# Kernel optimization log

Measured on AMD Instinct MI355X. Metric: run time of the kernel, lower is better.

Reference implementation:

```python
import jax, jax.numpy as jnp
import numpy as np

EPS = 1e-6
NEG = -10000.0
B, T, V, D, H, L, F = 2, 1024, 32000, 1024, 16, 4, 2730
DH = D // H
SCALE = 1.0 / np.sqrt(DH)


def alibi_slopes(n_head):
    # standard ALiBi geometric slopes (n_head is a power of 2 here)
    start = 2.0 ** (-8.0 / n_head)
    return jnp.asarray([start ** (i + 1) for i in range(n_head)], dtype=jnp.float32)


def rational_softmax(x, eps=EPS):
    # exp-free softmax: Pade [0/2] rational surrogate of exp on shifted (<=0) scores
    s = x - jnp.max(x, axis=-1, keepdims=True)
    num = 1.0 / (1.0 - s + 0.5 * s * s)
    return num / (jnp.sum(num, axis=-1, keepdims=True) + eps)


def me_norm(x, w, eps=EPS):
    # mean-error norm: x / (mean|x| + eps) * w
    return x / (jnp.mean(jnp.abs(x), axis=-1, keepdims=True) + eps) * w


def setup_inputs() -> dict:
    key = jax.random.key(0)
    ks = jax.random.split(key, 9)
    std = 0.02
    return {
        "input_ids": jax.random.randint(ks[0], (B, T), 0, V),
        "embed_w":   jax.random.normal(ks[1], (V, D), jnp.float32) * std,  # tied with head
        "qkv_w":     jax.random.normal(ks[2], (L, 3 * D, D), jnp.float32) * std,
        "out_w":     jax.random.normal(ks[3], (L, D, D), jnp.float32) * std,
        "gate_w":    jax.random.normal(ks[4], (L, 2 * F, D), jnp.float32) * std,
        "wout_w":    jax.random.normal(ks[5], (L, D, F), jnp.float32) * std,
        "norm1_w":   jnp.ones((L, D), jnp.float32),
        "norm2_w":   jnp.ones((L, D), jnp.float32),
        "normf_w":   jnp.ones((D,), jnp.float32),
    }


def _forward(input_ids, embed_w, qkv_w, out_w, gate_w, wout_w, norm1_w, norm2_w, normf_w):
    slopes = alibi_slopes(H)                       # [H]
    pos = jnp.arange(T)
    rel = jnp.abs(pos[:, None] - pos[None, :]).astype(jnp.float32)  # [T,T]
    alibi = -rel[None] * slopes[:, None, None]     # [H,T,T]
    causal = jnp.triu(jnp.ones((T, T), bool), k=1) # future positions

    x = embed_w[input_ids]                         # [B,T,D]

    def block(x, p):
        w_qkv, w_out, w_gate, w_wout, n1, n2 = p
        h = me_norm(x, n1)
        qkv = (h @ w_qkv.T).reshape(B, T, 3, H, DH).transpose(2, 0, 3, 1, 4)
        q, k, v = qkv[0], qkv[1], qkv[2]           # [B,H,T,DH]
        scores = jnp.einsum('bhtd,bhsd->bhts', q, k) * SCALE + alibi
        scores = jnp.where(causal[None, None], NEG, scores)
        probs = rational_softmax(scores)
        o = jnp.einsum('bhts,bhsd->bhtd', probs, v)
        o = o.transpose(0, 2, 1, 3).reshape(B, T, D)
        x = x + o @ w_out.T
        h = me_norm(x, n2)
        gv = h @ w_gate.T                           # [B,T,2F]
        gate, val = gv[..., :F], gv[..., F:]
        sigma = 0.5 * (gate / (jnp.abs(gate) + 1.0) + 1.0)  # rational sigmoid
        x = x + (gate * sigma * val) @ w_wout.T
        return x, None

    x, _ = jax.lax.scan(block, x, (qkv_w, out_w, gate_w, wout_w, norm1_w, norm2_w))
    x = me_norm(x, normf_w)
    logits = x @ embed_w.T                          # tied head, [B,T,V]
    return logits


def reference(input_ids, embed_w, qkv_w, out_w, gate_w, wout_w, norm1_w, norm2_w, normf_w):
    return _forward(input_ids, embed_w, qkv_w, out_w, gate_w, wout_w, norm1_w, norm2_w, normf_w)
```

## Files before the change

### kernel.cpp

```cpp
#include <hip/hip_runtime.h>
#include <math.h>

typedef __attribute__((ext_vector_type(8))) short bf16x8;
typedef __attribute__((ext_vector_type(4))) float f32x4;

namespace {
constexpr int Bc = 2, Tc = 1024, Dc = 1024, Hc = 16, Fc = 2730;
constexpr int Fp = 2752;
constexpr int Gp = 5504;
constexpr int Mc = Bc * Tc;
constexpr float EPSc = 1e-6f;
constexpr float NEGc = -10000.0f;
constexpr float SCALEc = 0.125f;
}

__device__ __forceinline__ unsigned short f2b(float f) {
    unsigned int u = __float_as_uint(f);
    u += 0x7FFFu + ((u >> 16) & 1u);
    return (unsigned short)(u >> 16);
}

__global__ void k_embed(const int* __restrict__ ids, const float* __restrict__ ew,
                        float* __restrict__ x) {
    int row = blockIdx.x;
    int id = ids[row];
    const float4* src = (const float4*)(ew + (size_t)id * Dc);
    float4* dst = (float4*)(x + (size_t)row * Dc);
    dst[threadIdx.x] = src[threadIdx.x];
}

__global__ void k_conv(const float* __restrict__ in, unsigned short* __restrict__ out) {
    size_t i = ((size_t)blockIdx.x * 256 + threadIdx.x) * 4;
    float4 v = *(const float4*)(in + i);
    ushort4 o;
    o.x = f2b(v.x); o.y = f2b(v.y); o.z = f2b(v.z); o.w = f2b(v.w);
    *(ushort4*)(out + i) = o;
}

__global__ void k_conv_gate_ilv(const float* __restrict__ in, unsigned short* __restrict__ out) {
    int r = blockIdx.x;
    int c = threadIdx.x * 4;
    ushort4 o;
    if (r < 2 * Fc) {
        int src = (r >> 1) + (r & 1) * Fc;
        float4 v = *(const float4*)(in + (size_t)src * Dc + c);
        o.x = f2b(v.x); o.y = f2b(v.y); o.z = f2b(v.z); o.w = f2b(v.w);
    } else {
        o.x = o.y = o.z = o.w = 0;
    }
    *(ushort4*)(out + (size_t)r * Dc + c) = o;
}

__global__ void k_conv_padk(const float* __restrict__ in, unsigned short* __restrict__ out) {
    int r = blockIdx.x;
    for (int c = threadIdx.x; c < Fp; c += 256) {
        float v = (c < Fc) ? in[(size_t)r * Fc + c] : 0.0f;
        out[(size_t)r * Fp + c] = f2b(v);
    }
}

__global__ void k_menorm_b(const float* __restrict__ x, const float* __restrict__ w,
                           unsigned short* __restrict__ out) {
    int row = blockIdx.x;
    float4 v = ((const float4*)(x + (size_t)row * Dc))[threadIdx.x];
    float s = fabsf(v.x) + fabsf(v.y) + fabsf(v.z) + fabsf(v.w);
#pragma unroll
    for (int m = 32; m >= 1; m >>= 1) s += __shfl_xor(s, m);
    __shared__ float ws4[4];
    if ((threadIdx.x & 63) == 0) ws4[threadIdx.x >> 6] = s;
    __syncthreads();
    float tot = ws4[0] + ws4[1] + ws4[2] + ws4[3];
    float inv = 1.0f / (tot / (float)Dc + EPSc);
    float4 wv = ((const float4*)w)[threadIdx.x];
    ushort4 o;
    o.x = f2b(v.x * inv * wv.x);
    o.y = f2b(v.y * inv * wv.y);
    o.z = f2b(v.z * inv * wv.z);
    o.w = f2b(v.w * inv * wv.w);
    ((ushort4*)(out + (size_t)row * Dc))[threadIdx.x] = o;
}

template <int MODE, int BM>
__global__ __launch_bounds__(256) void k_mfma_gemm(
    const unsigned short* __restrict__ A, const unsigned short* __restrict__ Bw,
    const float* __restrict__ Res, float* __restrict__ C,
    unsigned short* __restrict__ U0, unsigned short* __restrict__ U1,
    unsigned short* __restrict__ U2, int N, int K) {
    constexpr int MFR = BM / 32;
    __shared__ __align__(16) unsigned short As[BM * 64];
    __shared__ __align__(16) unsigned short Bs[128 * 64];
    const int tid = threadIdx.x;
    const int lane = tid & 63;
    const int wid = tid >> 6;
    const int wr = wid >> 1, wc = wid & 1;
    const int l15 = lane & 15, g = lane >> 4;

    const int nwg = gridDim.x * gridDim.y;
    int w = blockIdx.y * gridDim.x + blockIdx.x;
    int f = (nwg & 7) ? w : ((w & 7) * (nwg >> 3) + (w >> 3));
    const int bm = (f % gridDim.x) * BM, bn = (f / gridDim.x) * 128;

    f32x4 acc[MFR][4] = {};

    const int nk = K >> 6;
    for (int kt = 0; kt < nk; ++kt) {
        const int k0 = kt << 6;
#pragma unroll
        for (int it = 0; it < MFR; ++it) {
            int ci = it * 256 + tid;
            int r = ci >> 3;
            int sc = (ci & 7) ^ (r & 7);
            __builtin_amdgcn_global_load_lds(
                (const __attribute__((address_space(1))) void*)(A + (size_t)(bm + r) * K + k0 + sc * 8),
                (__attribute__((address_space(3))) void*)(As + ci * 8), 16, 0, 0);
        }
#pragma unroll
        for (int it = 0; it < 4; ++it) {
            int ci = it * 256 + tid;
            int r = ci >> 3;
            int sc = (ci & 7) ^ (r & 7);
            __builtin_amdgcn_global_load_lds(
                (const __attribute__((address_space(1))) void*)(Bw + (size_t)(bn + r) * K + k0 + sc * 8),
                (__attribute__((address_space(3))) void*)(Bs + ci * 8), 16, 0, 0);
        }
        __syncthreads();
#pragma unroll
        for (int kk = 0; kk < 2; ++kk) {
            bf16x8 af[MFR], bfr[4];
            const int kc = kk * 4 + g;
#pragma unroll
            for (int m = 0; m < MFR; ++m) {
                int row = wr * (BM / 2) + m * 16 + l15;
                af[m] = *(const bf16x8*)&As[(row * 8 + (kc ^ (row & 7))) * 8];
            }
#pragma unroll
            for (int n = 0; n < 4; ++n) {
                int col = wc * 64 + n * 16 + l15;
                bfr[n] = *(const bf16x8*)&Bs[(col * 8 + (kc ^ (col & 7))) * 8];
            }
#pragma unroll
            for (int m = 0; m < MFR; ++m)
#pragma unroll
                for (int n = 0; n < 4; ++n)
                    acc[m][n] = __builtin_amdgcn_mfma_f32_16x16x32_bf16(af[m], bfr[n], acc[m][n], 0, 0, 0);
        }
        __syncthreads();
    }

#pragma unroll
    for (int m = 0; m < MFR; ++m) {
        int row0 = bm + wr * (BM / 2) + m * 16 + (g << 2);
#pragma unroll
        for (int n = 0; n < 4; ++n) {
            int col = bn + wc * 64 + n * 16 + l15;
            if constexpr (MODE == 0 || MODE == 1) {
#pragma unroll
                for (int j = 0; j < 4; ++j) {
                    size_t idx = (size_t)(row0 + j) * N + col;
                    float v = acc[m][n][j];
                    if (MODE == 1) v += Res[idx];
                    C[idx] = v;
                }
            } else if constexpr (MODE == 2) {
                if (col < 2048) {
                    unsigned short* dst = (col < 1024) ? U0 : U1;
                    int hh = (col & 1023) >> 6, dh = col & 63;
#pragma unroll
                    for (int j = 0; j < 4; ++j) {
                        int row = row0 + j;
                        int b = row >> 10, t = row & 1023;
                        dst[((size_t)((b * Hc + hh) * Tc + t)) * 64 + dh] = f2b(acc[m][n][j]);
                    }
                } else {
                    int hh = (col >> 6) & 15, dh = col & 63;
                    int b = row0 >> 10, t = row0 & 1023;
                    ushort4 o4;
                    o4.x = f2b(acc[m][n][0]); o4.y = f2b(acc[m][n][1]);
                    o4.z = f2b(acc[m][n][2]); o4.w = f2b(acc[m][n][3]);
                    *(ushort4*)&U2[((size_t)((b * Hc + hh) * 64 + dh)) * Tc + t] = o4;
                }
            } else {
                float pv[4];
#pragma unroll
                for (int j = 0; j < 4; ++j) pv[j] = __shfl_xor(acc[m][n][j], 1);
                if ((l15 & 1) == 0) {
                    int fq = col >> 1;
#pragma unroll
                    for (int j = 0; j < 4; ++j) {
                        float gate = acc[m][n][j], val = pv[j];
                        float sigma = 0.5f * (gate / (fabsf(gate) + 1.0f) + 1.0f);
                        U0[(size_t)(row0 + j) * Fp + fq] = f2b(gate * sigma * val);
                    }
                }
            }
        }
    }
}

__global__ __launch_bounds__(512, 2) void k_gemm_8ph(
    const unsigned short* __restrict__ A, const unsigned short* __restrict__ Bw,
    float* __restrict__ C, int N, int K) {
    __shared__ __align__(16) unsigned short As[2][256 * 64];
    __shared__ __align__(16) unsigned short Bs[2][256 * 64];
    const int tid = threadIdx.x;
    const int lane = tid & 63, wid = tid >> 6;
    const int wm = wid >> 2, wn = wid & 3;
    const int l15 = lane & 15, g = lane >> 4;

    const int bm = blockIdx.x * 256;
    const int bn = blockIdx.y * 256;

    const int nk = K >> 6;
    f32x4 acc[8][4] = {};

#define STAGE8(buf, kt)                                                                          \
    {                                                                                            \
        _Pragma("unroll") for (int it = 0; it < 4; ++it) {                                       \
            int ci = it * 512 + tid;                                                             \
            int r = ci >> 3, c = (ci & 7) ^ (r & 7);                                             \
            __builtin_amdgcn_global_load_lds(                                                    \
                (const __attribute__((address_space(1))) void*)(A + (size_t)(bm + r) * K + (kt) * 64 + c * 8), \
                (__attribute__((address_space(3))) void*)(&As[buf][ci * 8]), 16, 0, 0);          \
        }                                                                                        \
        _Pragma("unroll") for (int it = 0; it < 4; ++it) {                                       \
            int ci = it * 512 + tid;                                                             \
            int r = ci >> 3, c = (ci & 7) ^ (r & 7);                                             \
            __builtin_amdgcn_global_load_lds(                                                    \
                (const __attribute__((address_space(1))) void*)(Bw + (size_t)(bn + r) * K + (kt) * 64 + c * 8), \
                (__attribute__((address_space(3))) void*)(&Bs[buf][ci * 8]), 16, 0, 0);          \
        }                                                                                        \
    }

    STAGE8(0, 0);
    STAGE8(1, 1);
    asm volatile("s_waitcnt vmcnt(8)" ::: "memory");
    __builtin_amdgcn_s_barrier();

    for (int kt = 0; kt < nk; ++kt) {
        const int buf = kt & 1;
        const unsigned short* Ab = As[buf];
        const unsigned short* Bb = Bs[buf];
        bf16x8 bfr[4][2];
#pragma unroll
        for (int n = 0; n < 4; ++n) {
            int col = wn * 64 + n * 16 + l15;
#pragma unroll
            for (int kk = 0; kk < 2; ++kk) {
                int kc = kk * 4 + g;
                bfr[n][kk] = *(const bf16x8*)&Bb[(col * 8 + (kc ^ (col & 7))) * 8];
            }
        }
        bf16x8 af[4][2][2];
#pragma unroll
        for (int p = 0; p < 4; ++p)
#pragma unroll
            for (int le = 0; le < 2; ++le) {
                int row = wm * 128 + (p * 2 + le) * 16 + l15;
#pragma unroll
                for (int kk = 0; kk < 2; ++kk) {
                    int kc = kk * 4 + g;
                    af[p][le][kk] = *(const bf16x8*)&Ab[(row * 8 + (kc ^ (row & 7))) * 8];
                }
            }
        __builtin_amdgcn_s_setprio(1);
#pragma unroll
        for (int p = 0; p < 3; ++p)
#pragma unroll
            for (int kk = 0; kk < 2; ++kk)
#pragma unroll
                for (int le = 0; le < 2; ++le)
#pragma unroll
                    for (int n = 0; n < 4; ++n)
                        acc[p * 2 + le][n] = __builtin_amdgcn_mfma_f32_16x16x32_bf16(
                            af[p][le][kk], bfr[n][kk], acc[p * 2 + le][n], 0, 0, 0);
        __builtin_amdgcn_s_setprio(0);
        asm volatile("s_waitcnt lgkmcnt(0)" ::: "memory");
        __builtin_amdgcn_s_barrier();
        if (kt + 2 < nk) STAGE8(buf, kt + 2);
        __builtin_amdgcn_s_setprio(1);
#pragma unroll
        for (int kk = 0; kk < 2; ++kk)
#pragma unroll
            for (int le = 0; le < 2; ++le)
#pragma unroll
                for (int n = 0; n < 4; ++n)
                    acc[6 + le][n] = __builtin_amdgcn_mfma_f32_16x16x32_bf16(
                        af[3][le][kk], bfr[n][kk], acc[6 + le][n], 0, 0, 0);
        __builtin_amdgcn_s_setprio(0);
        if (kt + 2 < nk) {
            asm volatile("s_waitcnt vmcnt(8)" ::: "memory");
        } else {
            asm volatile("s_waitcnt vmcnt(0)" ::: "memory");
        }
        __builtin_amdgcn_s_barrier();
    }
#undef STAGE8

#pragma unroll
    for (int m = 0; m < 8; ++m) {
        int row0 = bm + wm * 128 + m * 16 + (g << 2);
#pragma unroll
        for (int n = 0; n < 4; ++n) {
            int col = bn + wn * 64 + n * 16 + l15;
#pragma unroll
            for (int j = 0; j < 4; ++j)
                C[(size_t)(row0 + j) * N + col] = acc[m][n][j];
        }
    }
}

__global__ __launch_bounds__(256) void k_attn_mfma(
    const unsigned short* __restrict__ Qh, const unsigned short* __restrict__ Kh,
    const unsigned short* __restrict__ Vt, unsigned short* __restrict__ o) {
    const int d0 = blockIdx.x;
    const int r0 = d0 & 255;
    const int slot = d0 >> 8;
    const int bh = r0 >> 3;
    const int e = r0 & 7;
    const int bx = slot ? (15 - e) : e;
    const int q0 = bx * 64;
    const int b = bh >> 4, h = bh & 15;
    const float slope = exp2f(-0.5f * (float)(h + 1));

    __shared__ __align__(16) unsigned short Ks[128 * 64];
    __shared__ __align__(16) unsigned short Vs[64 * 128];
    __shared__ __align__(16) unsigned short Ps[4][16 * 128];

    const int tid = threadIdx.x, lane = tid & 63, wid = tid >> 6;
    const int q0w = q0 + wid * 16;
    const int l15 = lane & 15, g = lane >> 4;

    const unsigned short* qbase = Qh + ((size_t)(bh * Tc + q0w + l15)) * 64 + g * 8;
    bf16x8 qf[2];
    qf[0] = *(const bf16x8*)qbase;
    qf[1] = *(const bf16x8*)(qbase + 32);

    const int nt = (bx >> 1) + 1;

#define STAGE_K128(it)                                                                           \
    {                                                                                            \
        _Pragma("unroll") for (int i = 0; i < 4; ++i) {                                          \
            int ci = i * 256 + tid;                                                              \
            int r = ci >> 3, sc = (ci & 7) ^ (r & 7);                                            \
            __builtin_amdgcn_global_load_lds(                                                    \
                (const __attribute__((address_space(1))) void*)(Kh + ((size_t)(bh * Tc + (it) * 128 + r)) * 64 + sc * 8), \
                (__attribute__((address_space(3))) void*)(Ks + ci * 8), 16, 0, 0);               \
        }                                                                                        \
    }
#define STAGE_V128(it)                                                                           \
    {                                                                                            \
        _Pragma("unroll") for (int i = 0; i < 4; ++i) {                                          \
            int ci = i * 256 + tid;                                                              \
            int dh = ci >> 4, th = (ci >> 3) & 1, c = ci & 7;                                    \
            int sc = c ^ (dh & 7);                                                               \
            __builtin_amdgcn_global_load_lds(                                                    \
                (const __attribute__((address_space(1))) void*)(Vt + ((size_t)(bh * 64 + dh)) * Tc + (it) * 128 + th * 64 + sc * 8), \
                (__attribute__((address_space(3))) void*)(Vs + ci * 8), 16, 0, 0);               \
        }                                                                                        \
    }

    f32x4 mx = {-3e38f, -3e38f, -3e38f, -3e38f};
    for (int it = 0; it < nt; ++it) {
        const int st = it * 128;
        __syncthreads();
        STAGE_K128(it);
        __syncthreads();
#pragma unroll
        for (int si = 0; si < 8; ++si) {
            f32x4 d = {0.f, 0.f, 0.f, 0.f};
            int r2 = si * 16 + l15;
#pragma unroll
            for (int kc = 0; kc < 2; ++kc) {
                int c2 = kc * 4 + g;
                bf16x8 bk = *(const bf16x8*)&Ks[(r2 * 8 + (c2 ^ (r2 & 7))) * 8];
                d = __builtin_amdgcn_mfma_f32_16x16x32_bf16(qf[kc], bk, d, 0, 0, 0);
            }
            int s = st + r2;
#pragma unroll
            for (int j = 0; j < 4; ++j) {
                int t = q0w + g * 4 + j;
                float scv = (s <= t) ? d[j] * SCALEc - slope * (float)(t - s) : -3e38f;
                mx[j] = fmaxf(mx[j], scv);
            }
        }
    }
#pragma unroll
    for (int m = 8; m >= 1; m >>= 1)
#pragma unroll
        for (int j = 0; j < 4; ++j) mx[j] = fmaxf(mx[j], __shfl_xor(mx[j], m));

    f32x4 sum = {0.f, 0.f, 0.f, 0.f};
    f32x4 oacc[4] = {};
    for (int it = 0; it < nt; ++it) {
        const int st = it * 128;
        __syncthreads();
        STAGE_K128(it);
        STAGE_V128(it);
        __syncthreads();
#pragma unroll
        for (int si = 0; si < 8; ++si) {
            f32x4 d = {0.f, 0.f, 0.f, 0.f};
            int sl = si * 16 + l15;
#pragma unroll
            for (int kc = 0; kc < 2; ++kc) {
                int c2 = kc * 4 + g;
                bf16x8 bk = *(const bf16x8*)&Ks[(sl * 8 + (c2 ^ (sl & 7))) * 8];
                d = __builtin_amdgcn_mfma_f32_16x16x32_bf16(qf[kc], bk, d, 0, 0, 0);
            }
            int s = st + sl;
            int chunk = sl >> 3, coff = sl & 7;
#pragma unroll
            for (int j = 0; j < 4; ++j) {
                int t = q0w + g * 4 + j;
                int q = g * 4 + j;
                unsigned short pb = 0;
                if (s <= t) {
                    float sv = d[j] * SCALEc - slope * (float)(t - s) - mx[j];
                    float num = __builtin_amdgcn_rcpf(fmaf(0.5f * sv, sv, 1.0f - sv));
                    sum[j] += num;
                    pb = f2b(num);
                }
                Ps[wid][q * 128 + ((chunk & 8) | ((chunk & 7) ^ (q & 7))) * 8 + coff] = pb;
            }
        }
        __syncthreads();
#pragma unroll
        for (int kc2 = 0; kc2 < 4; ++kc2) {
            int c2 = kc2 * 4 + g;
            bf16x8 pa = *(const bf16x8*)&Ps[wid][(l15 * 16 + ((c2 & 8) | ((c2 & 7) ^ (l15 & 7)))) * 8];
#pragma unroll
            for (int n = 0; n < 4; ++n) {
                int r2 = n * 16 + l15;
                bf16x8 vb = *(const bf16x8*)&Vs[(r2 * 16 + ((c2 & 8) | ((c2 & 7) ^ (r2 & 7)))) * 8];
                oacc[n] = __builtin_amdgcn_mfma_f32_16x16x32_bf16(pa, vb, oacc[n], 0, 0, 0);
            }
        }
    }
#undef STAGE_K128
#undef STAGE_V128
#pragma unroll
    for (int m = 8; m >= 1; m >>= 1)
#pragma unroll
        for (int j = 0; j < 4; ++j) sum[j] += __shfl_xor(sum[j], m);

#pragma unroll
    for (int j = 0; j < 4; ++j) {
        int t = q0w + g * 4 + j;
        float svm = NEGc - mx[j];
        float mnum = __builtin_amdgcn_rcpf(fmaf(0.5f * svm, svm, 1.0f - svm));
        float inv = __builtin_amdgcn_rcpf(sum[j] + (float)(Tc - 1 - t) * mnum + EPSc);
#pragma unroll
        for (int n = 0; n < 4; ++n) {
            o[((size_t)(b * Tc + t)) * Dc + h * 64 + n * 16 + l15] = f2b(oacc[n][j] * inv);
        }
    }
}

extern "C" void kernel_launch(void* const* d_in, const int* in_sizes, int n_in,
                              void* d_out, int out_size, void* d_ws, size_t ws_size,
                              hipStream_t stream) {
    const int* ids = (const int*)d_in[0];
    const float* embed_w = (const float*)d_in[1];
    const float* qkv_w = (const float*)d_in[2];
    const float* out_w = (const float*)d_in[3];
    const float* gate_w = (const float*)d_in[4];
    const float* wout_w = (const float*)d_in[5];
    const float* n1 = (const float*)d_in[6];
    const float* n2 = (const float*)d_in[7];
    const float* nf = (const float*)d_in[8];
    float* outp = (float*)d_out;

    char* ws = (char*)d_ws;
    float* x = (float*)(ws + 0);
    unsigned short* h = (unsigned short*)(ws + 8388608);
    unsigned short* Qh = (unsigned short*)(ws + 12582912);
    unsigned short* Kh = (unsigned short*)(ws + 16777216);
    unsigned short* Vt = (unsigned short*)(ws + 20971520);
    unsigned short* g = (unsigned short*)(ws + 25165824);
    unsigned short* w1 = (unsigned short*)(ws + 36438016);
    unsigned short* wo_b = (unsigned short*)(ws + 42729472);
    unsigned short* wg_b = (unsigned short*)(ws + 44826624);
    unsigned short* emb_b = (unsigned short*)(ws + 12582912);

    dim3 blk(256);

    k_embed<<<dim3(Mc), blk, 0, stream>>>(ids, embed_w, x);

    for (int l = 0; l < 4; l++) {
        const float* wq = qkv_w + (size_t)l * 3 * Dc * Dc;
        const float* wo = out_w + (size_t)l * Dc * Dc;
        const float* wg = gate_w + (size_t)l * 2 * Fc * Dc;
        const float* ww = wout_w + (size_t)l * Dc * Fc;

        k_conv<<<dim3(3072), blk, 0, stream>>>(wq, w1);
        k_conv<<<dim3(1024), blk, 0, stream>>>(wo, wo_b);
        k_conv_gate_ilv<<<dim3(Gp), blk, 0, stream>>>(wg, wg_b);

        k_menorm_b<<<dim3(Mc), blk, 0, stream>>>(x, n1 + (size_t)l * Dc, h);
        k_mfma_gemm<2, 128><<<dim3(16, 24), blk, 0, stream>>>(h, w1, nullptr, nullptr, Qh, Kh, Vt, 3 * Dc, Dc);
        k_conv_padk<<<dim3(1024), blk, 0, stream>>>(ww, w1);
        k_attn_mfma<<<dim3(512), blk, 0, stream>>>(Qh, Kh, Vt, h);
        k_mfma_gemm<1, 64><<<dim3(32, 8), blk, 0, stream>>>(h, wo_b, x, x, nullptr, nullptr, nullptr, Dc, Dc);
        k_menorm_b<<<dim3(Mc), blk, 0, stream>>>(x, n2 + (size_t)l * Dc, h);
        k_mfma_gemm<3, 128><<<dim3(16, Gp / 128), blk, 0, stream>>>(h, wg_b, nullptr, nullptr, g, nullptr, nullptr, Gp, Dc);
        k_mfma_gemm<1, 64><<<dim3(32, 8), blk, 0, stream>>>(g, w1, x, x, nullptr, nullptr, nullptr, Dc, Fp);
    }

    k_menorm_b<<<dim3(Mc), blk, 0, stream>>>(x, nf, h);
    k_conv<<<dim3(32000), blk, 0, stream>>>(embed_w, emb_b);
    k_gemm_8ph<<<dim3(8, 125), dim3(512), 0, stream>>>(h, emb_b, outp, 32000, Dc);
}
```

Measured before the change: 1.009 ms.

## Double-buffer MFMA GEMM LDS tiles and fuse per-layer weight conversions

The MFMA GEMM now uses two LDS buffers, prefetching tile k+2 while computing tile k. It uses manual vmcnt waits, raw barriers and s_setprio around the MFMA blocks to overlap global-to-LDS loads with compute. The four per-layer weight conversion kernels are merged into one launch writing to a new ww_b workspace region, which cuts launch overhead. LDS use per block doubles, which may lower occupancy, and the hand-tuned waitcnt values must match the number of loads issued.

Measured after the change: 947.2 us. 6.1% less time.

```diff
diff --git a/kernel.cpp b/kernel.cpp
--- a/kernel.cpp
+++ b/kernel.cpp
@@ -37,25 +37,38 @@
     *(ushort4*)(out + i) = o;
 }
 
-__global__ void k_conv_gate_ilv(const float* __restrict__ in, unsigned short* __restrict__ out) {
+__global__ void k_conv_layer(const float* __restrict__ wq, const float* __restrict__ wo,
+                             const float* __restrict__ wg, const float* __restrict__ ww,
+                             unsigned short* __restrict__ wq_b, unsigned short* __restrict__ wo_b,
+                             unsigned short* __restrict__ wg_b, unsigned short* __restrict__ ww_b) {
     int r = blockIdx.x;
-    int c = threadIdx.x * 4;
-    ushort4 o;
-    if (r < 2 * Fc) {
-        int src = (r >> 1) + (r & 1) * Fc;
-        float4 v = *(const float4*)(in + (size_t)src * Dc + c);
-        o.x = f2b(v.x); o.y = f2b(v.y); o.z = f2b(v.z); o.w = f2b(v.w);
+    int c4 = threadIdx.x * 4;
+    if (r < 3072) {
+        float4 v = *(const float4*)(wq + (size_t)r * Dc + c4);
+        ushort4 o; o.x = f2b(v.x); o.y = f2b(v.y); o.z = f2b(v.z); o.w = f2b(v.w);
+        *(ushort4*)(wq_b + (size_t)r * Dc + c4) = o;
+    } else if (r < 4096) {
+        int rr = r - 3072;
+        float4 v = *(const float4*)(wo + (size_t)rr * Dc + c4);
+        ushort4 o; o.x = f2b(v.x); o.y = f2b(v.y); o.z = f2b(v.z); o.w = f2b(v.w);
+        *(ushort4*)(wo_b + (size_t)rr * Dc + c4) = o;
+    } else if (r < 9600) {
+        int rr = r - 4096;
+        ushort4 o;
+        if (rr < 2 * Fc) {
+            int src = (rr >> 1) + (rr & 1) * Fc;
+            float4 v = *(const float4*)(wg + (size_t)src * Dc + c4);
+            o.x = f2b(v.x); o.y = f2b(v.y); o.z = f2b(v.z); o.w = f2b(v.w);
+        } else {
+            o.x = o.y = o.z = o.w = 0;
+        }
+        *(ushort4*)(wg_b + (size_t)rr * Dc + c4) = o;
     } else {
-        o.x = o.y = o.z = o.w = 0;
-    }
-    *(ushort4*)(out + (size_t)r * Dc + c) = o;
-}
-
-__global__ void k_conv_padk(const float* __restrict__ in, unsigned short* __restrict__ out) {
-    int r = blockIdx.x;
-    for (int c = threadIdx.x; c < Fp; c += 256) {
-        float v = (c < Fc) ? in[(size_t)r * Fc + c] : 0.0f;
-        out[(size_t)r * Fp + c] = f2b(v);
+        int rr = r - 9600;
+        for (int c = threadIdx.x; c < Fp; c += 256) {
+            float v = (c < Fc) ? ww[(size_t)rr * Fc + c] : 0.0f;
+            ww_b[(size_t)rr * Fp + c] = f2b(v);
+        }
     }
 }
 
@@ -87,8 +100,8 @@
     unsigned short* __restrict__ U0, unsigned short* __restrict__ U1,
     unsigned short* __restrict__ U2, int N, int K) {
     constexpr int MFR = BM / 32;
-    __shared__ __align__(16) unsigned short As[BM * 64];
-    __shared__ __align__(16) unsigned short Bs[128 * 64];
+    __shared__ __align__(16) unsigned short As[2][BM * 64];
+    __shared__ __align__(16) unsigned short Bs[2][128 * 64];
     const int tid = threadIdx.x;
     const int lane = tid & 63;
     const int wid = tid >> 6;
@@ -101,51 +114,84 @@
     const int bm = (f % gridDim.x) * BM, bn = (f / gridDim.x) * 128;
 
     f32x4 acc[MFR][4] = {};
-
     const int nk = K >> 6;
+
+#define STAGEL(buf, kt)                                                                          \
+    {                                                                                            \
+        _Pragma("unroll") for (int it = 0; it < MFR; ++it) {                                     \
+            int ci = it * 256 + tid;                                                             \
+            int r = ci >> 3, sc = (ci & 7) ^ (r & 7);                                            \
+            __builtin_amdgcn_global_load_lds(                                                    \
+                (const __attribute__((address_space(1))) void*)(A + (size_t)(bm + r) * K + (kt) * 64 + sc * 8), \
+                (__attribute__((address_space(3))) void*)(&As[buf][ci * 8]), 16, 0, 0);          \
+        }                                                                                        \
+        _Pragma("unroll") for (int it = 0; it < 4; ++it) {                                       \
+            int ci = it * 256 + tid;                                                             \
+            int r = ci >> 3, sc = (ci & 7) ^ (r & 7);                                            \
+            __builtin_amdgcn_global_load_lds(                                                    \
+                (const __attribute__((address_space(1))) void*)(Bw + (size_t)(bn + r) * K + (kt) * 64 + sc * 8), \
+                (__attribute__((address_space(3))) void*)(&Bs[buf][ci * 8]), 16, 0, 0);          \
+        }                                                                                        \
+    }
+
+    STAGEL(0, 0);
+    STAGEL(1, 1);
+    if constexpr (BM == 128) { asm volatile("s_waitcnt vmcnt(8)" ::: "memory"); }
+    else                     { asm volatile("s_waitcnt vmcnt(6)" ::: "memory"); }
+    __builtin_amdgcn_s_barrier();
+
     for (int kt = 0; kt < nk; ++kt) {
-        const int k0 = kt << 6;
-#pragma unroll
-        for (int it = 0; it < MFR; ++it) {
-            int ci = it * 256 + tid;
-            int r = ci >> 3;
-            int sc = (ci & 7) ^ (r & 7);
-            __builtin_amdgcn_global_load_lds(
-                (const __attribute__((address_space(1))) void*)(A + (size_t)(bm + r) * K + k0 + sc * 8),
-                (__attribute__((address_space(3))) void*)(As + ci * 8), 16, 0, 0);
-        }
-#pragma unroll
-        for (int it = 0; it < 4; ++it) {
-            int ci = it * 256 + tid;
-            int r = ci >> 3;
-            int sc = (ci & 7) ^ (r & 7);
-            __builtin_amdgcn_global_load_lds(
-                (const __attribute__((address_space(1))) void*)(Bw + (size_t)(bn + r) * K + k0 + sc * 8),
-                (__attribute__((address_space(3))) void*)(Bs + ci * 8), 16, 0, 0);
-        }
-        __syncthreads();
-#pragma unroll
-        for (int kk = 0; kk < 2; ++kk) {
-            bf16x8 af[MFR], bfr[4];
-            const int kc = kk * 4 + g;
-#pragma unroll
-            for (int m = 0; m < MFR; ++m) {
-                int row = wr * (BM / 2) + m * 16 + l15;
-                af[m] = *(const bf16x8*)&As[(row * 8 + (kc ^ (row & 7))) * 8];
-            }
-#pragma unroll
-            for (int n = 0; n < 4; ++n) {
-                int col = wc * 64 + n * 16 + l15;
-                bfr[n] = *(const bf16x8*)&Bs[(col * 8 + (kc ^ (col & 7))) * 8];
-            }
-#pragma unroll
-            for (int m = 0; m < MFR; ++m)
+        const int buf = kt & 1;
+        const unsigned short* Ab = As[buf];
+        const unsigned short* Bb = Bs[buf];
+        bf16x8 bfr[4][2];
+#pragma unroll
+        for (int n = 0; n < 4; ++n) {
+            int col = wc * 64 + n * 16 + l15;
+#pragma unroll
+            for (int kk = 0; kk < 2; ++kk) {
+                int kc = kk * 4 + g;
+                bfr[n][kk] = *(const bf16x8*)&Bb[(col * 8 + (kc ^ (col & 7))) * 8];
+            }
+        }
+        bf16x8 af[MFR][2];
+#pragma unroll
+        for (int m = 0; m < MFR; ++m) {
+            int row = wr * (BM / 2) + m * 16 + l15;
+#pragma unroll
+            for (int kk = 0; kk < 2; ++kk) {
+                int kc = kk * 4 + g;
+                af[m][kk] = *(const bf16x8*)&Ab[(row * 8 + (kc ^ (row & 7))) * 8];
+            }
+        }
+        __builtin_amdgcn_s_setprio(1);
+#pragma unroll
+        for (int m = 0; m < MFR - 1; ++m)
+#pragma unroll
+            for (int kk = 0; kk < 2; ++kk)
 #pragma unroll
                 for (int n = 0; n < 4; ++n)
-                    acc[m][n] = __builtin_amdgcn_mfma_f32_16x16x32_bf16(af[m], bfr[n], acc[m][n], 0, 0, 0);
-        }
-        __syncthreads();
-    }
+                    acc[m][n] = __builtin_amdgcn_mfma_f32_16x16x32_bf16(af[m][kk], bfr[n][kk], acc[m][n], 0, 0, 0);
+        __builtin_amdgcn_s_setprio(0);
+        asm volatile("s_waitcnt lgkmcnt(0)" ::: "memory");
+        __builtin_amdgcn_s_barrier();
+        if (kt + 2 < nk) STAGEL(buf, kt + 2);
+        __builtin_amdgcn_s_setprio(1);
+#pragma unroll
+        for (int kk = 0; kk < 2; ++kk)
+#pragma unroll
+            for (int n = 0; n < 4; ++n)
+                acc[MFR - 1][n] = __builtin_amdgcn_mfma_f32_16x16x32_bf16(af[MFR - 1][kk], bfr[n][kk], acc[MFR - 1][n], 0, 0, 0);
+        __builtin_amdgcn_s_setprio(0);
+        if (kt + 2 < nk) {
+            if constexpr (BM == 128) { asm volatile("s_waitcnt vmcnt(8)" ::: "memory"); }
+            else                     { asm volatile("s_waitcnt vmcnt(6)" ::: "memory"); }
+        } else {
+            asm volatile("s_waitcnt vmcnt(0)" ::: "memory");
+        }
+        __builtin_amdgcn_s_barrier();
+    }
+#undef STAGEL
 
 #pragma unroll
     for (int m = 0; m < MFR; ++m) {
@@ -480,6 +526,7 @@
     unsigned short* w1 = (unsigned short*)(ws + 36438016);
     unsigned short* wo_b = (unsigned short*)(ws + 42729472);
     unsigned short* wg_b = (unsigned short*)(ws + 44826624);
+    unsigned short* ww_b = (unsigned short*)(ws + 56098816);
     unsigned short* emb_b = (unsigned short*)(ws + 12582912);
 
     dim3 blk(256);
@@ -492,18 +539,15 @@
         const float* wg = gate_w + (size_t)l * 2 * Fc * Dc;
         const float* ww = wout_w + (size_t)l * Dc * Fc;
 
-        k_conv<<<dim3(3072), blk, 0, stream>>>(wq, w1);
-        k_conv<<<dim3(1024), blk, 0, stream>>>(wo, wo_b);
-        k_conv_gate_ilv<<<dim3(Gp), blk, 0, stream>>>(wg, wg_b);
+        k_conv_layer<<<dim3(10624), blk, 0, stream>>>(wq, wo, wg, ww, w1, wo_b, wg_b, ww_b);
 
         k_menorm_b<<<dim3(Mc), blk, 0, stream>>>(x, n1 + (size_t)l * Dc, h);
         k_mfma_gemm<2, 128><<<dim3(16, 24), blk, 0, stream>>>(h, w1, nullptr, nullptr, Qh, Kh, Vt, 3 * Dc, Dc);
-        k_conv_padk<<<dim3(1024), blk, 0, stream>>>(ww, w1);
         k_attn_mfma<<<dim3(512), blk, 0, stream>>>(Qh, Kh, Vt, h);
         k_mfma_gemm<1, 64><<<dim3(32, 8), blk, 0, stream>>>(h, wo_b, x, x, nullptr, nullptr, nullptr, Dc, Dc);
         k_menorm_b<<<dim3(Mc), blk, 0, stream>>>(x, n2 + (size_t)l * Dc, h);
         k_mfma_gemm<3, 128><<<dim3(16, Gp / 128), blk, 0, stream>>>(h, wg_b, nullptr, nullptr, g, nullptr, nullptr, Gp, Dc);
-        k_mfma_gemm<1, 64><<<dim3(32, 8), blk, 0, stream>>>(g, w1, x, x, nullptr, nullptr, nullptr, Dc, Fp);
+        k_mfma_gemm<1, 64><<<dim3(32, 8), blk, 0, stream>>>(g, ww_b, x, x, nullptr, nullptr, nullptr, Dc, Fp);
     }
 
     k_menorm_b<<<dim3(Mc), blk, 0, stream>>>(x, nf, h);
```
